# Kernel tuning notes

Hardware: AMD Instinct MI355X
Metric: run time of the kernel (lower is better)

The kernel has to match this reference:

```python
import jax, jax.numpy as jnp
import numpy as np


def _rope_cache(seq_len, head_dim):
    half = head_dim // 2
    inv_freq = 1.0 / (10000.0 ** (jnp.arange(half, dtype=jnp.float32) / half))
    ang = jnp.arange(seq_len, dtype=jnp.float32)[:, None] * inv_freq[None, :]  # [S, half]
    return jnp.cos(ang), jnp.sin(ang)


def _apply_rope(x, cos, sin):
    # x: [B,H,S,D], interleaved pairs (even=x1, odd=x2)
    b, h, s, d = x.shape
    xp = x.reshape(b, h, s, d // 2, 2)
    x1, x2 = xp[..., 0], xp[..., 1]
    c = cos[:s][None, None]
    sn = sin[:s][None, None]
    o1 = x1 * c - x2 * sn
    o2 = x1 * sn + x2 * c
    return jnp.stack([o1, o2], axis=-1).reshape(b, h, s, d)


def setup_inputs() -> dict:
    key = jax.random.key(0)
    ks = jax.random.split(key, 5)
    B, N, D = 2, 2048, 2048
    sc = 0.02
    return {
        "x": jax.random.normal(ks[0], (B, N, D), jnp.float32),
        "wq": jax.random.normal(ks[1], (D, D), jnp.float32) * sc,
        "wk": jax.random.normal(ks[2], (D, D), jnp.float32) * sc,
        "wv": jax.random.normal(ks[3], (D, D), jnp.float32) * sc,
        "wo": jax.random.normal(ks[4], (D, D), jnp.float32) * sc,
    }


def reference(x, wq, wk, wv, wo):
    H = 16
    B, N, D = x.shape
    dk = D // H
    # torch nn.Linear: y = x @ W^T
    def proj(w):
        return (x @ w.T).reshape(B, N, H, dk).transpose(0, 2, 1, 3)  # [B,H,N,dk]
    Q, K, V = proj(wq), proj(wk), proj(wv)
    cos, sin = _rope_cache(N, dk)
    Q = _apply_rope(Q, cos, sin)
    K = _apply_rope(K, cos, sin)
    scores = jnp.einsum('bhnd,bhmd->bhnm', Q, K) / jnp.sqrt(jnp.float32(dk))
    causal = jnp.tril(jnp.ones((N, N), dtype=bool))
    scores = jnp.where(causal[None, None], scores, -jnp.inf)
    attn = jax.nn.softmax(scores, axis=-1)
    out = jnp.einsum('bhnm,bhmd->bhnd', attn, V)
    out = out.transpose(0, 2, 1, 3).reshape(B, N, D)
    return out @ wo.T, K, V
```

## Files before the change

kernel.cpp:

```cpp
#include <hip/hip_runtime.h>
#include <stdint.h>

typedef __bf16 bf16x8 __attribute__((ext_vector_type(8)));
typedef float f32x4 __attribute__((ext_vector_type(4)));

#define DEV __device__ __forceinline__
#define CAST_G(p) (const __attribute__((address_space(1))) unsigned int*)(p)
#define CAST_L(p) (__attribute__((address_space(3))) unsigned int*)(p)

constexpr int SEQ = 2048;
constexpr int DIM = 2048;
constexpr int NH  = 16;
constexpr int DK  = 128;
constexpr int BATCH = 2;
constexpr size_t TSZ = (size_t)BATCH * SEQ * DIM;
constexpr size_t WSZ = (size_t)DIM * DIM;
constexpr float ATTN_SCALE = 0.08838834764831845f;

DEV unsigned short f2bf(float f) {
  unsigned int u = __float_as_uint(f);
  unsigned int r = (u + 0x7fffu + ((u >> 16) & 1u)) >> 16;
  return (unsigned short)r;
}

__global__ __launch_bounds__(256)
void cvt_f32_bf16(const float* __restrict__ src, unsigned short* __restrict__ dst,
                  int n8) {
  int i = blockIdx.x * 256 + threadIdx.x;
  if (i >= n8) return;
  float4 a = *reinterpret_cast<const float4*>(src + (size_t)i * 8);
  float4 b = *reinterpret_cast<const float4*>(src + (size_t)i * 8 + 4);
  unsigned short o[8];
  o[0] = f2bf(a.x); o[1] = f2bf(a.y); o[2] = f2bf(a.z); o[3] = f2bf(a.w);
  o[4] = f2bf(b.x); o[5] = f2bf(b.y); o[6] = f2bf(b.z); o[7] = f2bf(b.w);
  *reinterpret_cast<uint4*>(dst + (size_t)i * 8) = *reinterpret_cast<const uint4*>(o);
}

template <int MODE>
__global__ __launch_bounds__(256, 2)
void gemm_rope(const unsigned short* __restrict__ A,
               const unsigned short* __restrict__ W,
               unsigned short* __restrict__ Db,
               float* __restrict__ Df) {
  __shared__ __align__(16) unsigned short As[128 * 64];
  __shared__ __align__(16) unsigned short Bs[128 * 64];

  const int t = threadIdx.x;
  const int lane = t & 63;
  const int wid = t >> 6;
  const int wr = (wid >> 1) << 6;
  const int wc = (wid & 1) << 6;
  const int l16 = lane & 15, lg = lane >> 4;
  const int row0 = blockIdx.y * 128;
  const int col0 = blockIdx.x * 128;

  const int srow = t >> 3;
  const int scol = ((t & 7) ^ (srow & 7)) << 3;
  const unsigned short* Asrc = A + (size_t)(row0 + srow) * DIM + scol;
  const unsigned short* Wsrc = W + (size_t)(col0 + srow) * DIM + scol;

  f32x4 acc[4][4] = {};

  for (int k0 = 0; k0 < DIM; k0 += 64) {
    __syncthreads();
#pragma unroll
    for (int i = 0; i < 4; ++i) {
      __builtin_amdgcn_global_load_lds(CAST_G(Asrc + (size_t)i * 32 * DIM + k0),
                                       CAST_L(As + i * 2048 + wid * 512), 16, 0, 0);
      __builtin_amdgcn_global_load_lds(CAST_G(Wsrc + (size_t)i * 32 * DIM + k0),
                                       CAST_L(Bs + i * 2048 + wid * 512), 16, 0, 0);
    }
    __syncthreads();
#pragma unroll
    for (int ks = 0; ks < 2; ++ks) {
      bf16x8 af[4], bfr[4];
#pragma unroll
      for (int i = 0; i < 4; ++i) {
        int ra = wr + i * 16 + l16;
        af[i] = *reinterpret_cast<const bf16x8*>(&As[ra * 64 + (((ks * 4 + lg) ^ (ra & 7)) << 3)]);
        int rb = wc + i * 16 + l16;
        bfr[i] = *reinterpret_cast<const bf16x8*>(&Bs[rb * 64 + (((ks * 4 + lg) ^ (rb & 7)) << 3)]);
      }
#pragma unroll
      for (int i = 0; i < 4; ++i)
#pragma unroll
        for (int j = 0; j < 4; ++j)
          acc[i][j] = __builtin_amdgcn_mfma_f32_16x16x32_bf16(af[i], bfr[j], acc[i][j], 0, 0, 0);
    }
  }

  if (MODE == 0) {
#pragma unroll
    for (int i = 0; i < 4; ++i)
#pragma unroll
      for (int j = 0; j < 4; ++j) {
        int colg = col0 + wc + j * 16 + l16;
#pragma unroll
        for (int r = 0; r < 4; ++r) {
          int rowg = row0 + wr + i * 16 + lg * 4 + r;
          Df[(size_t)rowg * DIM + colg] = acc[i][j][r];
        }
      }
  } else {
#pragma unroll
    for (int j = 0; j < 4; ++j) {
      int colg = col0 + wc + j * 16 + l16;
      int jj = (colg >> 1) & 63;
      float invf = __expf((float)jj * -0.14391156831212787f);
#pragma unroll
      for (int i = 0; i < 4; ++i) {
#pragma unroll
        for (int r = 0; r < 4; ++r) {
          int rowg = row0 + wr + i * 16 + lg * 4 + r;
          float v = acc[i][j][r];
          float outv;
          if (MODE == 1 || MODE == 2) {
            float p = __shfl_xor(v, 1, 64);
            int pos = rowg & (SEQ - 1);
            float ang = (float)pos * invf;
            float sn, cs;
            __sincosf(ang, &sn, &cs);
            outv = (colg & 1) ? fmaf(p, sn, v * cs) : fmaf(v, cs, -(p * sn));
          } else {
            outv = v;
          }
          int b = rowg >> 11, pos = rowg & (SEQ - 1);
          int h = colg >> 7, d = colg & (DK - 1);
          size_t idx = (((size_t)(b * NH + h)) * SEQ + pos) * DK + d;
          if (MODE == 1) Db[idx] = f2bf(outv);
          if (MODE == 2) { Df[idx] = outv; Db[idx] = f2bf(outv); }
          if (MODE == 3) Df[idx] = outv;
        }
      }
    }
  }
}

__global__ __launch_bounds__(256, 2)
void vtrans(const float* __restrict__ V, unsigned short* __restrict__ VT) {
  __shared__ float vs[64 * 128];
  const int t = threadIdx.x;
  const int bh = blockIdx.y;
  const int p0 = blockIdx.x * 64;
  const float* src = V + ((size_t)bh * SEQ + p0) * DK;
#pragma unroll
  for (int s = 0; s < 8; ++s) {
    int id = s * 256 + t;
    *reinterpret_cast<float4*>(&vs[id * 4]) = *reinterpret_cast<const float4*>(&src[id * 4]);
  }
  __syncthreads();
  const int w = t >> 6, l = t & 63;
  unsigned short* dstb = VT + (size_t)bh * DK * SEQ + p0;
#pragma unroll
  for (int it = 0; it < 4; ++it) {
    int d = w * 32 + (it & 1) * 16 + (l & 15);
    int kc = (it >> 1) * 4 + (l >> 4);
    unsigned short tmp[8];
#pragma unroll
    for (int j = 0; j < 8; ++j) tmp[j] = f2bf(vs[(kc * 8 + j) * DK + d]);
    *reinterpret_cast<uint4*>(&dstb[(size_t)d * SEQ + kc * 8]) =
        *reinterpret_cast<const uint4*>(tmp);
  }
}

struct __align__(16) AttnSmem {
  unsigned short Qs[128 * 128];
  unsigned short Ks[64 * 128];
  unsigned short Vts[128 * 64];
  unsigned short Ps[4 * 32 * 64];
};

__global__ __launch_bounds__(256, 2)
void attn_fused(const unsigned short* __restrict__ Q,
                const unsigned short* __restrict__ K,
                const unsigned short* __restrict__ VT,
                unsigned short* __restrict__ AO) {
  __shared__ AttnSmem sm;
  const int t = threadIdx.x;
  const int lane = t & 63;
  const int wid = t >> 6;
  const int l16 = lane & 15, lg = lane >> 4;

  const int lin = (int)(blockIdx.x + gridDim.x * blockIdx.y);
  const int xcd = lin & 7;
  const int idx = lin >> 3;
  const int bh = xcd * 4 + (idx >> 4);
  const int qt = 15 - (idx & 15);
  const int b = bh >> 4, h = bh & 15;
  const int q0 = qt * 128;

  const unsigned short* Qbase = Q + ((size_t)bh * SEQ + q0) * DK;
  const unsigned short* Kbase = K + (size_t)bh * SEQ * DK;
  const unsigned short* VTbase = VT + (size_t)bh * DK * SEQ;

#pragma unroll
  for (int s = 0; s < 8; ++s) {
    int id = s * 256 + t;
    int r = id >> 4, c = id & 15;
    uint4 v = *reinterpret_cast<const uint4*>(Qbase + (size_t)r * DK + (c << 3));
    *reinterpret_cast<uint4*>(&sm.Qs[r * 128 + ((c ^ (r & 7)) << 3)]) = v;
  }

  f32x4 accO[2][8] = {};
  float mrun[2][4], lrun[2][4];
#pragma unroll
  for (int mi = 0; mi < 2; ++mi)
#pragma unroll
    for (int r = 0; r < 4; ++r) { mrun[mi][r] = -INFINITY; lrun[mi][r] = 0.f; }

  const int nkv = (q0 + 128) / 64;

  uint4 pk[4], pv[4];
#pragma unroll
  for (int s = 0; s < 4; ++s) {
    int id = s * 256 + t;
    int rk = id >> 4, ck = id & 15;
    pk[s] = *reinterpret_cast<const uint4*>(Kbase + (size_t)rk * DK + (ck << 3));
    int rv = id >> 3, cv = id & 7;
    pv[s] = *reinterpret_cast<const uint4*>(VTbase + (size_t)rv * SEQ + (cv << 3));
  }

  for (int kt = 0; kt < nkv; ++kt) {
    const int key0 = kt * 64;
    __syncthreads();
#pragma unroll
    for (int s = 0; s < 4; ++s) {
      int id = s * 256 + t;
      int rk = id >> 4, ck = id & 15;
      *reinterpret_cast<uint4*>(&sm.Ks[rk * 128 + ((ck ^ (rk & 7)) << 3)]) = pk[s];
      int rv = id >> 3, cv = id & 7;
      *reinterpret_cast<uint4*>(&sm.Vts[rv * 64 + ((cv ^ (rv & 7)) << 3)]) = pv[s];
    }
    __syncthreads();
    if (kt + 1 < nkv) {
      const int kn = key0 + 64;
#pragma unroll
      for (int s = 0; s < 4; ++s) {
        int id = s * 256 + t;
        int rk = id >> 4, ck = id & 15;
        pk[s] = *reinterpret_cast<const uint4*>(Kbase + (size_t)(kn + rk) * DK + (ck << 3));
        int rv = id >> 3, cv = id & 7;
        pv[s] = *reinterpret_cast<const uint4*>(VTbase + (size_t)rv * SEQ + kn + (cv << 3));
      }
    }

    f32x4 sf[2][4] = {};
#pragma unroll
    for (int ks = 0; ks < 4; ++ks) {
      bf16x8 aq[2], bk[4];
#pragma unroll
      for (int mi = 0; mi < 2; ++mi) {
        int r = wid * 32 + mi * 16 + l16;
        aq[mi] = *reinterpret_cast<const bf16x8*>(
            &sm.Qs[r * 128 + (((ks * 4 + lg) ^ (r & 7)) << 3)]);
      }
#pragma unroll
      for (int nj = 0; nj < 4; ++nj) {
        int r = nj * 16 + l16;
        bk[nj] = *reinterpret_cast<const bf16x8*>(
            &sm.Ks[r * 128 + (((ks * 4 + lg) ^ (r & 7)) << 3)]);
      }
#pragma unroll
      for (int mi = 0; mi < 2; ++mi)
#pragma unroll
        for (int nj = 0; nj < 4; ++nj)
          sf[mi][nj] = __builtin_amdgcn_mfma_f32_16x16x32_bf16(aq[mi], bk[nj], sf[mi][nj], 0, 0, 0);
    }

    const int qwbase = q0 + wid * 32;
    const bool need_mask = (key0 + 63) > qwbase;
#pragma unroll
    for (int mi = 0; mi < 2; ++mi)
#pragma unroll
      for (int nj = 0; nj < 4; ++nj) {
        int kcol = key0 + nj * 16 + l16;
#pragma unroll
        for (int r = 0; r < 4; ++r) {
          float v = sf[mi][nj][r] * ATTN_SCALE;
          if (need_mask) {
            int qrow = qwbase + mi * 16 + lg * 4 + r;
            if (kcol > qrow) v = -INFINITY;
          }
          sf[mi][nj][r] = v;
        }
      }

#pragma unroll
    for (int mi = 0; mi < 2; ++mi) {
      float alpha[4];
#pragma unroll
      for (int r = 0; r < 4; ++r) {
        float m0 = fmaxf(fmaxf(sf[mi][0][r], sf[mi][1][r]),
                         fmaxf(sf[mi][2][r], sf[mi][3][r]));
#pragma unroll
        for (int off = 1; off < 16; off <<= 1)
          m0 = fmaxf(m0, __shfl_xor(m0, off, 64));
        float mn = fmaxf(mrun[mi][r], m0);
        alpha[r] = __expf(mrun[mi][r] - mn);
        mrun[mi][r] = mn;
      }
      float rs[4] = {0.f, 0.f, 0.f, 0.f};
#pragma unroll
      for (int nj = 0; nj < 4; ++nj) {
        int colb = nj * 16 + l16;
        int ch = colb >> 3, cb = colb & 7;
#pragma unroll
        for (int r = 0; r < 4; ++r) {
          float p = __expf(sf[mi][nj][r] - mrun[mi][r]);
          rs[r] += p;
          int prow = mi * 16 + lg * 4 + r;
          sm.Ps[wid * 2048 + prow * 64 + ((ch ^ (prow & 7)) << 3) + cb] = f2bf(p);
        }
      }
#pragma unroll
      for (int r = 0; r < 4; ++r) {
        float s0 = rs[r];
#pragma unroll
        for (int off = 1; off < 16; off <<= 1)
          s0 += __shfl_xor(s0, off, 64);
        lrun[mi][r] = lrun[mi][r] * alpha[r] + s0;
      }
#pragma unroll
      for (int dj = 0; dj < 8; ++dj)
#pragma unroll
        for (int r = 0; r < 4; ++r) accO[mi][dj][r] *= alpha[r];
    }

#pragma unroll
    for (int ks = 0; ks < 2; ++ks) {
      bf16x8 ap[2], bv[8];
#pragma unroll
      for (int mi = 0; mi < 2; ++mi) {
        int r = mi * 16 + l16;
        ap[mi] = *reinterpret_cast<const bf16x8*>(
            &sm.Ps[wid * 2048 + r * 64 + (((ks * 4 + lg) ^ (r & 7)) << 3)]);
      }
#pragma unroll
      for (int dj = 0; dj < 8; ++dj) {
        int r = dj * 16 + l16;
        bv[dj] = *reinterpret_cast<const bf16x8*>(
            &sm.Vts[r * 64 + (((ks * 4 + lg) ^ (r & 7)) << 3)]);
      }
#pragma unroll
      for (int mi = 0; mi < 2; ++mi)
#pragma unroll
        for (int dj = 0; dj < 8; ++dj)
          accO[mi][dj] = __builtin_amdgcn_mfma_f32_16x16x32_bf16(ap[mi], bv[dj], accO[mi][dj], 0, 0, 0);
    }
  }

  unsigned short* Pw = &sm.Ps[wid * 2048];
#pragma unroll
  for (int mi = 0; mi < 2; ++mi) {
    float inv[4];
#pragma unroll
    for (int r = 0; r < 4; ++r) inv[r] = 1.0f / lrun[mi][r];
#pragma unroll
    for (int dj = 0; dj < 8; ++dj)
#pragma unroll
      for (int r = 0; r < 4; ++r)
        Pw[(lg * 4 + r) * 128 + dj * 16 + l16] = f2bf(accO[mi][dj][r] * inv[r]);
#pragma unroll
    for (int ps = 0; ps < 4; ++ps) {
      int row = ps * 4 + lg;
      uint4 v = *reinterpret_cast<const uint4*>(&Pw[row * 128 + l16 * 8]);
      int qpos = q0 + wid * 32 + mi * 16 + row;
      *reinterpret_cast<uint4*>(
          &AO[((size_t)(b * SEQ + qpos)) * DIM + h * DK + l16 * 8]) = v;
    }
  }
}

extern "C" void kernel_launch(void* const* d_in, const int* in_sizes, int n_in,
                              void* d_out, int out_size, void* d_ws, size_t ws_size,
                              hipStream_t stream) {
  const float* x  = (const float*)d_in[0];
  const float* wq = (const float*)d_in[1];
  const float* wk = (const float*)d_in[2];
  const float* wv = (const float*)d_in[3];
  const float* wo = (const float*)d_in[4];

  float* outF = (float*)d_out;
  float* outK = outF + TSZ;
  float* outV = outF + 2 * TSZ;

  unsigned short* qb = (unsigned short*)outF;
  unsigned short* kb = qb + TSZ;

  unsigned short* xb  = (unsigned short*)d_ws;
  unsigned short* aop = xb + TSZ;
  unsigned short* wb  = xb + 2 * TSZ;
  unsigned short* vtb = xb;

  dim3 blk(256);
  dim3 ggrid(16, 32);
  const int cvtW = (int)(WSZ / 2048), n8W = (int)(WSZ / 8);

  cvt_f32_bf16<<<dim3((int)(TSZ / 2048)), blk, 0, stream>>>(x, xb, (int)(TSZ / 8));

  cvt_f32_bf16<<<dim3(cvtW), blk, 0, stream>>>(wq, wb, n8W);
  gemm_rope<1><<<ggrid, blk, 0, stream>>>(xb, wb, qb, nullptr);

  cvt_f32_bf16<<<dim3(cvtW), blk, 0, stream>>>(wk, wb, n8W);
  gemm_rope<2><<<ggrid, blk, 0, stream>>>(xb, wb, kb, outK);

  cvt_f32_bf16<<<dim3(cvtW), blk, 0, stream>>>(wv, wb, n8W);
  gemm_rope<3><<<ggrid, blk, 0, stream>>>(xb, wb, nullptr, outV);

  vtrans<<<dim3(32, 32), blk, 0, stream>>>(outV, vtb);

  attn_fused<<<dim3(16, 32), blk, 0, stream>>>(qb, kb, vtb, aop);

  cvt_f32_bf16<<<dim3(cvtW), blk, 0, stream>>>(wo, wb, n8W);
  gemm_rope<0><<<ggrid, blk, 0, stream>>>(aop, wb, nullptr, outF);
}
```

Measured before the change: 397.3 us.

## Restructure attention into 512-thread blocks processing paired causal query tiles

The attention kernel now uses 512 threads (8 waves, 16 query rows each) and each block processes two query tiles (qt and 15-qt) sequentially, balancing causal work across blocks. The grid is halved to 8x32 and the XCD-aware block remapping is removed. The epilogue staging reuses the Ks buffer, with extra barriers added around it. The aim is better load balance and less per-wave register pressure. The cost is fewer blocks (256) with one block per CU, which may reduce latency hiding and L2 locality.

New measurement: 358.3 us. -9.8%, faster.

```diff
diff --git a/kernel.cpp b/kernel.cpp
--- a/kernel.cpp
+++ b/kernel.cpp
@@ -167,10 +167,10 @@
   unsigned short Qs[128 * 128];
   unsigned short Ks[64 * 128];
   unsigned short Vts[128 * 64];
-  unsigned short Ps[4 * 32 * 64];
+  unsigned short Ps[8 * 16 * 64];
 };
 
-__global__ __launch_bounds__(256, 2)
+__global__ __launch_bounds__(512, 1)
 void attn_fused(const unsigned short* __restrict__ Q,
                 const unsigned short* __restrict__ K,
                 const unsigned short* __restrict__ VT,
@@ -180,124 +180,107 @@
   const int lane = t & 63;
   const int wid = t >> 6;
   const int l16 = lane & 15, lg = lane >> 4;
-
-  const int lin = (int)(blockIdx.x + gridDim.x * blockIdx.y);
-  const int xcd = lin & 7;
-  const int idx = lin >> 3;
-  const int bh = xcd * 4 + (idx >> 4);
-  const int qt = 15 - (idx & 15);
+  const int pj = blockIdx.x;
+  const int bh = blockIdx.y;
   const int b = bh >> 4, h = bh & 15;
-  const int q0 = qt * 128;
-
-  const unsigned short* Qbase = Q + ((size_t)bh * SEQ + q0) * DK;
+
   const unsigned short* Kbase = K + (size_t)bh * SEQ * DK;
   const unsigned short* VTbase = VT + (size_t)bh * DK * SEQ;
 
-#pragma unroll
-  for (int s = 0; s < 8; ++s) {
-    int id = s * 256 + t;
-    int r = id >> 4, c = id & 15;
-    uint4 v = *reinterpret_cast<const uint4*>(Qbase + (size_t)r * DK + (c << 3));
-    *reinterpret_cast<uint4*>(&sm.Qs[r * 128 + ((c ^ (r & 7)) << 3)]) = v;
-  }
-
-  f32x4 accO[2][8] = {};
-  float mrun[2][4], lrun[2][4];
-#pragma unroll
-  for (int mi = 0; mi < 2; ++mi)
-#pragma unroll
-    for (int r = 0; r < 4; ++r) { mrun[mi][r] = -INFINITY; lrun[mi][r] = 0.f; }
-
-  const int nkv = (q0 + 128) / 64;
-
-  uint4 pk[4], pv[4];
-#pragma unroll
-  for (int s = 0; s < 4; ++s) {
-    int id = s * 256 + t;
-    int rk = id >> 4, ck = id & 15;
-    pk[s] = *reinterpret_cast<const uint4*>(Kbase + (size_t)rk * DK + (ck << 3));
-    int rv = id >> 3, cv = id & 7;
-    pv[s] = *reinterpret_cast<const uint4*>(VTbase + (size_t)rv * SEQ + (cv << 3));
-  }
-
-  for (int kt = 0; kt < nkv; ++kt) {
-    const int key0 = kt * 64;
-    __syncthreads();
+  for (int half = 0; half < 2; ++half) {
+    const int qt = half ? pj : (15 - pj);
+    const int q0 = qt * 128;
+    const int nkv = 2 * (qt + 1);
+    const unsigned short* Qbase = Q + ((size_t)bh * SEQ + q0) * DK;
+
 #pragma unroll
     for (int s = 0; s < 4; ++s) {
-      int id = s * 256 + t;
+      int id = s * 512 + t;
+      int r = id >> 4, c = id & 15;
+      uint4 v = *reinterpret_cast<const uint4*>(Qbase + (size_t)r * DK + (c << 3));
+      *reinterpret_cast<uint4*>(&sm.Qs[r * 128 + ((c ^ (r & 7)) << 3)]) = v;
+    }
+
+    f32x4 accO[8] = {};
+    float mrun[4], lrun[4];
+#pragma unroll
+    for (int r = 0; r < 4; ++r) { mrun[r] = -INFINITY; lrun[r] = 0.f; }
+
+    uint4 pk[2], pv[2];
+#pragma unroll
+    for (int s = 0; s < 2; ++s) {
+      int id = s * 512 + t;
       int rk = id >> 4, ck = id & 15;
-      *reinterpret_cast<uint4*>(&sm.Ks[rk * 128 + ((ck ^ (rk & 7)) << 3)]) = pk[s];
+      pk[s] = *reinterpret_cast<const uint4*>(Kbase + (size_t)rk * DK + (ck << 3));
       int rv = id >> 3, cv = id & 7;
-      *reinterpret_cast<uint4*>(&sm.Vts[rv * 64 + ((cv ^ (rv & 7)) << 3)]) = pv[s];
-    }
-    __syncthreads();
-    if (kt + 1 < nkv) {
-      const int kn = key0 + 64;
-#pragma unroll
-      for (int s = 0; s < 4; ++s) {
-        int id = s * 256 + t;
+      pv[s] = *reinterpret_cast<const uint4*>(VTbase + (size_t)rv * SEQ + (cv << 3));
+    }
+
+    for (int kt = 0; kt < nkv; ++kt) {
+      const int key0 = kt * 64;
+      __syncthreads();
+#pragma unroll
+      for (int s = 0; s < 2; ++s) {
+        int id = s * 512 + t;
         int rk = id >> 4, ck = id & 15;
-        pk[s] = *reinterpret_cast<const uint4*>(Kbase + (size_t)(kn + rk) * DK + (ck << 3));
+        *reinterpret_cast<uint4*>(&sm.Ks[rk * 128 + ((ck ^ (rk & 7)) << 3)]) = pk[s];
         int rv = id >> 3, cv = id & 7;
-        pv[s] = *reinterpret_cast<const uint4*>(VTbase + (size_t)rv * SEQ + kn + (cv << 3));
-      }
-    }
-
-    f32x4 sf[2][4] = {};
-#pragma unroll
-    for (int ks = 0; ks < 4; ++ks) {
-      bf16x8 aq[2], bk[4];
-#pragma unroll
-      for (int mi = 0; mi < 2; ++mi) {
-        int r = wid * 32 + mi * 16 + l16;
-        aq[mi] = *reinterpret_cast<const bf16x8*>(
-            &sm.Qs[r * 128 + (((ks * 4 + lg) ^ (r & 7)) << 3)]);
-      }
-#pragma unroll
-      for (int nj = 0; nj < 4; ++nj) {
-        int r = nj * 16 + l16;
-        bk[nj] = *reinterpret_cast<const bf16x8*>(
-            &sm.Ks[r * 128 + (((ks * 4 + lg) ^ (r & 7)) << 3)]);
-      }
-#pragma unroll
-      for (int mi = 0; mi < 2; ++mi)
-#pragma unroll
-        for (int nj = 0; nj < 4; ++nj)
-          sf[mi][nj] = __builtin_amdgcn_mfma_f32_16x16x32_bf16(aq[mi], bk[nj], sf[mi][nj], 0, 0, 0);
-    }
-
-    const int qwbase = q0 + wid * 32;
-    const bool need_mask = (key0 + 63) > qwbase;
-#pragma unroll
-    for (int mi = 0; mi < 2; ++mi)
+        *reinterpret_cast<uint4*>(&sm.Vts[rv * 64 + ((cv ^ (rv & 7)) << 3)]) = pv[s];
+      }
+      __syncthreads();
+      if (kt + 1 < nkv) {
+        const int kn = key0 + 64;
+#pragma unroll
+        for (int s = 0; s < 2; ++s) {
+          int id = s * 512 + t;
+          int rk = id >> 4, ck = id & 15;
+          pk[s] = *reinterpret_cast<const uint4*>(Kbase + (size_t)(kn + rk) * DK + (ck << 3));
+          int rv = id >> 3, cv = id & 7;
+          pv[s] = *reinterpret_cast<const uint4*>(VTbase + (size_t)rv * SEQ + kn + (cv << 3));
+        }
+      }
+
+      f32x4 sf[4] = {};
+#pragma unroll
+      for (int ks = 0; ks < 4; ++ks) {
+        int ra = wid * 16 + l16;
+        bf16x8 aq = *reinterpret_cast<const bf16x8*>(
+            &sm.Qs[ra * 128 + (((ks * 4 + lg) ^ (ra & 7)) << 3)]);
+#pragma unroll
+        for (int nj = 0; nj < 4; ++nj) {
+          int rb = nj * 16 + l16;
+          bf16x8 bk = *reinterpret_cast<const bf16x8*>(
+              &sm.Ks[rb * 128 + (((ks * 4 + lg) ^ (rb & 7)) << 3)]);
+          sf[nj] = __builtin_amdgcn_mfma_f32_16x16x32_bf16(aq, bk, sf[nj], 0, 0, 0);
+        }
+      }
+
+      const int qwbase = q0 + wid * 16;
+      const bool need_mask = (key0 + 63) > qwbase;
 #pragma unroll
       for (int nj = 0; nj < 4; ++nj) {
         int kcol = key0 + nj * 16 + l16;
 #pragma unroll
         for (int r = 0; r < 4; ++r) {
-          float v = sf[mi][nj][r] * ATTN_SCALE;
+          float v = sf[nj][r] * ATTN_SCALE;
           if (need_mask) {
-            int qrow = qwbase + mi * 16 + lg * 4 + r;
+            int qrow = qwbase + lg * 4 + r;
             if (kcol > qrow) v = -INFINITY;
           }
-          sf[mi][nj][r] = v;
-        }
-      }
-
-#pragma unroll
-    for (int mi = 0; mi < 2; ++mi) {
+          sf[nj][r] = v;
+        }
+      }
+
       float alpha[4];
 #pragma unroll
       for (int r = 0; r < 4; ++r) {
-        float m0 = fmaxf(fmaxf(sf[mi][0][r], sf[mi][1][r]),
-                         fmaxf(sf[mi][2][r], sf[mi][3][r]));
+        float m0 = fmaxf(fmaxf(sf[0][r], sf[1][r]), fmaxf(sf[2][r], sf[3][r]));
 #pragma unroll
         for (int off = 1; off < 16; off <<= 1)
           m0 = fmaxf(m0, __shfl_xor(m0, off, 64));
-        float mn = fmaxf(mrun[mi][r], m0);
-        alpha[r] = __expf(mrun[mi][r] - mn);
-        mrun[mi][r] = mn;
+        float mn = fmaxf(mrun[r], m0);
+        alpha[r] = __expf(mrun[r] - mn);
+        mrun[r] = mn;
       }
       float rs[4] = {0.f, 0.f, 0.f, 0.f};
 #pragma unroll
@@ -306,10 +289,10 @@
         int ch = colb >> 3, cb = colb & 7;
 #pragma unroll
         for (int r = 0; r < 4; ++r) {
-          float p = __expf(sf[mi][nj][r] - mrun[mi][r]);
+          float p = __expf(sf[nj][r] - mrun[r]);
           rs[r] += p;
-          int prow = mi * 16 + lg * 4 + r;
-          sm.Ps[wid * 2048 + prow * 64 + ((ch ^ (prow & 7)) << 3) + cb] = f2bf(p);
+          int prow = lg * 4 + r;
+          sm.Ps[wid * 1024 + prow * 64 + ((ch ^ (prow & 7)) << 3) + cb] = f2bf(p);
         }
       }
 #pragma unroll
@@ -318,56 +301,46 @@
 #pragma unroll
         for (int off = 1; off < 16; off <<= 1)
           s0 += __shfl_xor(s0, off, 64);
-        lrun[mi][r] = lrun[mi][r] * alpha[r] + s0;
+        lrun[r] = lrun[r] * alpha[r] + s0;
       }
 #pragma unroll
       for (int dj = 0; dj < 8; ++dj)
 #pragma unroll
-        for (int r = 0; r < 4; ++r) accO[mi][dj][r] *= alpha[r];
-    }
-
-#pragma unroll
-    for (int ks = 0; ks < 2; ++ks) {
-      bf16x8 ap[2], bv[8];
-#pragma unroll
-      for (int mi = 0; mi < 2; ++mi) {
-        int r = mi * 16 + l16;
-        ap[mi] = *reinterpret_cast<const bf16x8*>(
-            &sm.Ps[wid * 2048 + r * 64 + (((ks * 4 + lg) ^ (r & 7)) << 3)]);
-      }
-#pragma unroll
-      for (int dj = 0; dj < 8; ++dj) {
-        int r = dj * 16 + l16;
-        bv[dj] = *reinterpret_cast<const bf16x8*>(
-            &sm.Vts[r * 64 + (((ks * 4 + lg) ^ (r & 7)) << 3)]);
-      }
-#pragma unroll
-      for (int mi = 0; mi < 2; ++mi)
-#pragma unroll
-        for (int dj = 0; dj < 8; ++dj)
-          accO[mi][dj] = __builtin_amdgcn_mfma_f32_16x16x32_bf16(ap[mi], bv[dj], accO[mi][dj], 0, 0, 0);
-    }
-  }
-
-  unsigned short* Pw = &sm.Ps[wid * 2048];
-#pragma unroll
-  for (int mi = 0; mi < 2; ++mi) {
+        for (int r = 0; r < 4; ++r) accO[dj][r] *= alpha[r];
+
+#pragma unroll
+      for (int ks = 0; ks < 2; ++ks) {
+        bf16x8 ap = *reinterpret_cast<const bf16x8*>(
+            &sm.Ps[wid * 1024 + l16 * 64 + (((ks * 4 + lg) ^ (l16 & 7)) << 3)]);
+#pragma unroll
+        for (int dj = 0; dj < 8; ++dj) {
+          int rv = dj * 16 + l16;
+          bf16x8 bv = *reinterpret_cast<const bf16x8*>(
+              &sm.Vts[rv * 64 + (((ks * 4 + lg) ^ (rv & 7)) << 3)]);
+          accO[dj] = __builtin_amdgcn_mfma_f32_16x16x32_bf16(ap, bv, accO[dj], 0, 0, 0);
+        }
+      }
+    }
+
+    __syncthreads();
+    unsigned short* Pw = sm.Ks + wid * 2048;
     float inv[4];
 #pragma unroll
-    for (int r = 0; r < 4; ++r) inv[r] = 1.0f / lrun[mi][r];
+    for (int r = 0; r < 4; ++r) inv[r] = 1.0f / lrun[r];
 #pragma unroll
     for (int dj = 0; dj < 8; ++dj)
 #pragma unroll
       for (int r = 0; r < 4; ++r)
-        Pw[(lg * 4 + r) * 128 + dj * 16 + l16] = f2bf(accO[mi][dj][r] * inv[r]);
+        Pw[(lg * 4 + r) * 128 + dj * 16 + l16] = f2bf(accO[dj][r] * inv[r]);
 #pragma unroll
     for (int ps = 0; ps < 4; ++ps) {
       int row = ps * 4 + lg;
       uint4 v = *reinterpret_cast<const uint4*>(&Pw[row * 128 + l16 * 8]);
-      int qpos = q0 + wid * 32 + mi * 16 + row;
+      int qpos = q0 + wid * 16 + row;
       *reinterpret_cast<uint4*>(
           &AO[((size_t)(b * SEQ + qpos)) * DIM + h * DK + l16 * 8]) = v;
     }
+    __syncthreads();
   }
 }
 
@@ -409,7 +382,7 @@
 
   vtrans<<<dim3(32, 32), blk, 0, stream>>>(outV, vtb);
 
-  attn_fused<<<dim3(16, 32), blk, 0, stream>>>(qb, kb, vtb, aop);
+  attn_fused<<<dim3(8, 32), dim3(512), 0, stream>>>(qb, kb, vtb, aop);
 
   cvt_f32_bf16<<<dim3(cvtW), blk, 0, stream>>>(wo, wb, n8W);
   gemm_rope<0><<<ggrid, blk, 0, stream>>>(aop, wb, nullptr, outF);
```
